# Performance work log

Measured on AMD Instinct MI355X. Metric: run time of the kernel, lower is better.

Reference implementation:

```python
import jax, jax.numpy as jnp
import numpy as np

EPS = 1e-5  # BatchNorm eps


def _bn_relu(x, g, b, m, v):
    # inference-mode BatchNorm2d over channel axis 1, then ReLU
    inv = g / jnp.sqrt(v + EPS)
    return jax.nn.relu(x * inv[None, :, None, None] + (b - m * inv)[None, :, None, None])


def setup_inputs() -> dict:
    key = jax.random.key(0)
    ks = jax.random.split(key, 16)
    B, C, N, K = 8, 64, 16384, 16
    mlp = (128, 64, 64)
    inp = {
        "src_xyz": jax.random.normal(ks[0], (B, 3, N, K), jnp.float32),
        "tgt_xyz": jax.random.normal(ks[1], (B, 3, N), jnp.float32),
        "feature": jax.random.normal(ks[2], (B, C, N, K), jnp.float32),
    }
    prev = C + 4  # use_relation adds diff_xyz(3) + distance(1)
    i = 3
    for li, co in enumerate(mlp, 1):
        scale = (6.0 / (prev + co)) ** 0.5  # xavier_uniform
        inp[f"W{li}"] = jax.random.uniform(ks[i], (co, prev), jnp.float32, -scale, scale)
        inp[f"g{li}"] = jnp.ones((co,), jnp.float32)
        inp[f"b{li}"] = jnp.zeros((co,), jnp.float32)
        inp[f"m{li}"] = jnp.zeros((co,), jnp.float32)
        inp[f"v{li}"] = jnp.ones((co,), jnp.float32)
        prev = co
        i += 1
    return inp


def reference(src_xyz, tgt_xyz, feature,
              W1, g1, b1, m1, v1,
              W2, g2, b2, m2, v2,
              W3, g3, b3, m3, v3):
    d = 3  # NOTE: original code slices the NEIGHBOR dim to :3 (faithful quirk)
    diff = src_xyz[:, :, :, :d] - tgt_xyz[:, :, :, None]      # (B,3,N,3)
    dist = jnp.sum(diff * diff, axis=1, keepdims=True)        # (B,1,N,3)
    x = jnp.concatenate([feature[:, :, :, :d], diff, dist], axis=1)  # (B,C+4,N,3)
    for (W, g, b, m, v) in ((W1, g1, b1, m1, v1), (W2, g2, b2, m2, v2), (W3, g3, b3, m3, v3)):
        x = jnp.einsum('oc,bcnk->bonk', W, x)  # 1x1 conv (shared MLP)
        x = _bn_relu(x, g, b, m, v)
    return jnp.sum(x, axis=3)  # reduction='sum' over neighbor dim -> (B,64,N)
```

## Files before the change

### kernel.cpp

```cpp
#include <hip/hip_runtime.h>


typedef __attribute__((ext_vector_type(8))) short short8v;
typedef __attribute__((ext_vector_type(4))) float f32x4;

#define BN_EPS 1e-5f

__device__ __forceinline__ unsigned short f2bf(float f) {
    union { float f; unsigned u; } U; U.f = f;
    unsigned r = U.u + 0x7FFFu + ((U.u >> 16) & 1u);
    return (unsigned short)(r >> 16);
}

union FragU { uint4 u; short8v s; uint2 h[2]; };


__global__ __launch_bounds__(256) void fa_pack(
    const float* __restrict__ W1, const float* __restrict__ g1, const float* __restrict__ b1,
    const float* __restrict__ m1, const float* __restrict__ v1,
    const float* __restrict__ W2, const float* __restrict__ g2, const float* __restrict__ b2,
    const float* __restrict__ m2, const float* __restrict__ v2,
    const float* __restrict__ W3, const float* __restrict__ g3, const float* __restrict__ b3,
    const float* __restrict__ m3, const float* __restrict__ v3,
    char* __restrict__ ws)
{
    const int id = blockIdx.x * 256 + threadIdx.x;
    if (id < 1536) {
        const int lane = id & 63, frag = id >> 6;
        const int ct = frag / 3, ks = frag - 3 * ct;
        const int o  = ct * 16 + (lane & 15);
        const int kb = ks * 32 + (lane >> 4) * 8;
        unsigned short h[8];
        #pragma unroll
        for (int j = 0; j < 8; ++j) {
            const int k = kb + j;
            h[j] = (k < 68) ? f2bf(W1[o * 68 + k]) : (unsigned short)0;
        }
        uint4 pk;
        pk.x = h[0] | (h[1] << 16); pk.y = h[2] | (h[3] << 16);
        pk.z = h[4] | (h[5] << 16); pk.w = h[6] | (h[7] << 16);
        ((uint4*)ws)[id] = pk;
    } else if (id < 2560) {
        const int i2 = id - 1536;
        const int lane = i2 & 63, frag = i2 >> 6;
        const int o  = (frag >> 2) * 16 + (lane & 15);
        const int kb = (frag & 3) * 32 + (lane >> 4) * 8;
        unsigned short h[8];
        #pragma unroll
        for (int j = 0; j < 8; ++j) h[j] = f2bf(W2[o * 128 + kb + j]);
        uint4 pk;
        pk.x = h[0] | (h[1] << 16); pk.y = h[2] | (h[3] << 16);
        pk.z = h[4] | (h[5] << 16); pk.w = h[6] | (h[7] << 16);
        ((uint4*)(ws + 24576))[i2] = pk;
    } else if (id < 3072) {
        const int i3 = id - 2560;
        const int lane = i3 & 63, frag = i3 >> 6;
        const int o  = (frag >> 1) * 16 + (lane & 15);
        const int kb = (frag & 1) * 32 + (lane >> 4) * 8;
        unsigned short h[8];
        #pragma unroll
        for (int j = 0; j < 8; ++j) h[j] = f2bf(W3[o * 64 + kb + j]);
        uint4 pk;
        pk.x = h[0] | (h[1] << 16); pk.y = h[2] | (h[3] << 16);
        pk.z = h[4] | (h[5] << 16); pk.w = h[6] | (h[7] << 16);
        ((uint4*)(ws + 40960))[i3] = pk;
    } else if (id < 3200) {
        const int o = id - 3072;
        const float s = g1[o] * rsqrtf(v1[o] + BN_EPS);
        ((float*)(ws + 49152))[o] = s;
        ((float*)(ws + 49664))[o] = b1[o] - m1[o] * s;
    } else if (id < 3264) {
        const int o = id - 3200;
        const float s = g2[o] * rsqrtf(v2[o] + BN_EPS);
        ((float*)(ws + 50176))[o] = s;
        ((float*)(ws + 50432))[o] = b2[o] - m2[o] * s;
    } else if (id < 3328) {
        const int o = id - 3264;
        const float s = g3[o] * rsqrtf(v3[o] + BN_EPS);
        ((float*)(ws + 50688))[o] = s;
        ((float*)(ws + 50944))[o] = b3[o] - m3[o] * s;
    }
}

__global__ __launch_bounds__(256, 3) void fa_mfma(
    const float* __restrict__ src, const float* __restrict__ tgt,
    const float* __restrict__ feat,
    const char* __restrict__ ws, float* __restrict__ out)
{
    constexpr int N = 16384;
    __shared__ unsigned short SM[192 * 136];
    #define X0V(r, c) SM[(r) * 72 + (c)]
    #define X1V(r, c) SM[(r) * 136 + (c)]

    const int t  = threadIdx.x;
    const int b  = blockIdx.x >> 8;
    const int n0 = (blockIdx.x & 255) << 6;

    {
        const int p  = t & 63;
        const int cg = t >> 6;
        float4 fr[16];
        #pragma unroll
        for (int i = 0; i < 16; ++i) {
            const int c = cg * 16 + i;
            fr[i] = *(const float4*)(feat + ((size_t)(b * 64 + c) * N + n0 + p) * 16);
        }
        float rs0 = 0, rs1 = 0, rs2 = 0, rt0 = 0, rt1 = 0, rt2 = 0;
        const bool rel = t < 192;
        const int rp = t & 63, rk = t >> 6;
        if (rel) {
            const int n = n0 + rp;
            rs0 = src[((b * 3 + 0) * N + n) * 16 + rk]; rt0 = tgt[(b * 3 + 0) * N + n];
            rs1 = src[((b * 3 + 1) * N + n) * 16 + rk]; rt1 = tgt[(b * 3 + 1) * N + n];
            rs2 = src[((b * 3 + 2) * N + n) * 16 + rk]; rt2 = tgt[(b * 3 + 2) * N + n];
        }
        #pragma unroll
        for (int j = 0; j < 4; ++j) {
            const int c0 = cg * 16 + 4 * j;
            const float4 f0 = fr[4 * j + 0], f1 = fr[4 * j + 1];
            const float4 f2 = fr[4 * j + 2], f3 = fr[4 * j + 3];
            uint2 u0, u1, u2;
            u0.x = f2bf(f0.x) | (f2bf(f1.x) << 16); u0.y = f2bf(f2.x) | (f2bf(f3.x) << 16);
            u1.x = f2bf(f0.y) | (f2bf(f1.y) << 16); u1.y = f2bf(f2.y) | (f2bf(f3.y) << 16);
            u2.x = f2bf(f0.z) | (f2bf(f1.z) << 16); u2.y = f2bf(f2.z) | (f2bf(f3.z) << 16);
            *(uint2*)&X0V(0 * 64 + p, c0) = u0;
            *(uint2*)&X0V(1 * 64 + p, c0) = u1;
            *(uint2*)&X0V(2 * 64 + p, c0) = u2;
        }
        if (rel) {
            const float d0 = rs0 - rt0, d1 = rs1 - rt1, d2 = rs2 - rt2;
            const float ds = d0 * d0 + d1 * d1 + d2 * d2;
            uint2 wr; wr.x = f2bf(d0) | (f2bf(d1) << 16); wr.y = f2bf(d2) | (f2bf(ds) << 16);
            *(uint2*)&X0V(rk * 64 + rp, 64) = wr;
        }
    }
    __syncthreads();

    const int w = t >> 6, lane = t & 63, lo = lane & 15, hi = lane >> 4;

    const uint4*  w1f = (const uint4*)ws;
    const uint4*  w2f = (const uint4*)(ws + 24576);
    const uint4*  w3f = (const uint4*)(ws + 40960);
    const float*  s1w = (const float*)(ws + 49152);
    const float*  t1w = (const float*)(ws + 49664);
    const float*  s2w = (const float*)(ws + 50176);
    const float*  t2w = (const float*)(ws + 50432);
    const float*  s3w = (const float*)(ws + 50688);
    const float*  t3w = (const float*)(ws + 50944);

    short8v a1[3][3];
    #pragma unroll
    for (int k = 0; k < 3; ++k) {
        const int row = k * 64 + w * 16 + lo;
        a1[k][0] = *(const short8v*)&X0V(row, hi * 8);
        a1[k][1] = *(const short8v*)&X0V(row, 32 + hi * 8);
        FragU U; U.u.x = 0; U.u.y = 0; U.u.z = 0; U.u.w = 0;
        if (hi == 0) U.h[0] = *(const uint2*)&X0V(row, 64);
        a1[k][2] = U.s;
    }
    __syncthreads();

    #pragma unroll 2
    for (int ct = 0; ct < 8; ++ct) {
        FragU B0, B1, B2;
        B0.u = w1f[(ct * 3 + 0) * 64 + lane];
        B1.u = w1f[(ct * 3 + 1) * 64 + lane];
        B2.u = w1f[(ct * 3 + 2) * 64 + lane];
        const float sc = s1w[ct * 16 + lo];
        const float tb = t1w[ct * 16 + lo];
        #pragma unroll
        for (int k = 0; k < 3; ++k) {
            f32x4 acc = {0.f, 0.f, 0.f, 0.f};
            acc = __builtin_amdgcn_mfma_f32_16x16x32_bf16(a1[k][0], B0.s, acc, 0, 0, 0);
            acc = __builtin_amdgcn_mfma_f32_16x16x32_bf16(a1[k][1], B1.s, acc, 0, 0, 0);
            acc = __builtin_amdgcn_mfma_f32_16x16x32_bf16(a1[k][2], B2.s, acc, 0, 0, 0);
            const int rb = k * 64 + w * 16 + 4 * hi;
            #pragma unroll
            for (int j = 0; j < 4; ++j) {
                const float y = fmaxf(fmaf(sc, acc[j], tb), 0.f);
                X1V(rb + j, ct * 16 + lo) = f2bf(y);
            }
        }
    }

    short8v a2[3][4];
    #pragma unroll
    for (int k = 0; k < 3; ++k) {
        const int row = k * 64 + w * 16 + lo;
        #pragma unroll
        for (int ks = 0; ks < 4; ++ks)
            a2[k][ks] = *(const short8v*)&X1V(row, ks * 32 + hi * 8);
    }
    __syncthreads();

    #pragma unroll 2
    for (int ct = 0; ct < 4; ++ct) {
        FragU B0, B1, B2, B3;
        B0.u = w2f[(ct * 4 + 0) * 64 + lane];
        B1.u = w2f[(ct * 4 + 1) * 64 + lane];
        B2.u = w2f[(ct * 4 + 2) * 64 + lane];
        B3.u = w2f[(ct * 4 + 3) * 64 + lane];
        const float sc = s2w[ct * 16 + lo];
        const float tb = t2w[ct * 16 + lo];
        #pragma unroll
        for (int k = 0; k < 3; ++k) {
            f32x4 acc = {0.f, 0.f, 0.f, 0.f};
            acc = __builtin_amdgcn_mfma_f32_16x16x32_bf16(a2[k][0], B0.s, acc, 0, 0, 0);
            acc = __builtin_amdgcn_mfma_f32_16x16x32_bf16(a2[k][1], B1.s, acc, 0, 0, 0);
            acc = __builtin_amdgcn_mfma_f32_16x16x32_bf16(a2[k][2], B2.s, acc, 0, 0, 0);
            acc = __builtin_amdgcn_mfma_f32_16x16x32_bf16(a2[k][3], B3.s, acc, 0, 0, 0);
            const int rb = k * 64 + w * 16 + 4 * hi;
            #pragma unroll
            for (int j = 0; j < 4; ++j) {
                const float y = fmaxf(fmaf(sc, acc[j], tb), 0.f);
                X0V(rb + j, ct * 16 + lo) = f2bf(y);
            }
        }
    }

    short8v a3[3][2];
    #pragma unroll
    for (int k = 0; k < 3; ++k) {
        const int row = k * 64 + w * 16 + lo;
        a3[k][0] = *(const short8v*)&X0V(row, hi * 8);
        a3[k][1] = *(const short8v*)&X0V(row, 32 + hi * 8);
    }
    #pragma unroll 2
    for (int ct = 0; ct < 4; ++ct) {
        FragU B0, B1;
        B0.u = w3f[(ct * 2 + 0) * 64 + lane];
        B1.u = w3f[(ct * 2 + 1) * 64 + lane];
        const float sc = s3w[ct * 16 + lo];
        const float tb = t3w[ct * 16 + lo];
        f32x4 acc0 = {0.f, 0.f, 0.f, 0.f};
        f32x4 acc1 = {0.f, 0.f, 0.f, 0.f};
        f32x4 acc2 = {0.f, 0.f, 0.f, 0.f};
        acc0 = __builtin_amdgcn_mfma_f32_16x16x32_bf16(a3[0][0], B0.s, acc0, 0, 0, 0);
        acc0 = __builtin_amdgcn_mfma_f32_16x16x32_bf16(a3[0][1], B1.s, acc0, 0, 0, 0);
        acc1 = __builtin_amdgcn_mfma_f32_16x16x32_bf16(a3[1][0], B0.s, acc1, 0, 0, 0);
        acc1 = __builtin_amdgcn_mfma_f32_16x16x32_bf16(a3[1][1], B1.s, acc1, 0, 0, 0);
        acc2 = __builtin_amdgcn_mfma_f32_16x16x32_bf16(a3[2][0], B0.s, acc2, 0, 0, 0);
        acc2 = __builtin_amdgcn_mfma_f32_16x16x32_bf16(a3[2][1], B1.s, acc2, 0, 0, 0);
        float4 r;
        float* rp4 = &r.x;
        #pragma unroll
        for (int j = 0; j < 4; ++j) {
            rp4[j] = fmaxf(fmaf(sc, acc0[j], tb), 0.f)
                   + fmaxf(fmaf(sc, acc1[j], tb), 0.f)
                   + fmaxf(fmaf(sc, acc2[j], tb), 0.f);
        }
        float* op = out + (size_t)(b * 64 + ct * 16 + lo) * N + n0 + w * 16 + 4 * hi;
        *(float4*)op = r;
    }
    #undef X0V
    #undef X1V
}

extern "C" void kernel_launch(void* const* d_in, const int* in_sizes, int n_in,
                              void* d_out, int out_size, void* d_ws, size_t ws_size,
                              hipStream_t stream)
{
    const float* src  = (const float*)d_in[0];
    const float* tgt  = (const float*)d_in[1];
    const float* feat = (const float*)d_in[2];
    const float* W1 = (const float*)d_in[3];
    const float* g1 = (const float*)d_in[4];
    const float* b1 = (const float*)d_in[5];
    const float* m1 = (const float*)d_in[6];
    const float* v1 = (const float*)d_in[7];
    const float* W2 = (const float*)d_in[8];
    const float* g2 = (const float*)d_in[9];
    const float* b2 = (const float*)d_in[10];
    const float* m2 = (const float*)d_in[11];
    const float* v2 = (const float*)d_in[12];
    const float* W3 = (const float*)d_in[13];
    const float* g3 = (const float*)d_in[14];
    const float* b3 = (const float*)d_in[15];
    const float* m3 = (const float*)d_in[16];
    const float* v3 = (const float*)d_in[17];
    float* out = (float*)d_out;
    char* ws = (char*)d_ws;

    hipLaunchKernelGGL(fa_pack, dim3(13), dim3(256), 0, stream,
                       W1, g1, b1, m1, v1, W2, g2, b2, m2, v2, W3, g3, b3, m3, v3, ws);
    hipLaunchKernelGGL(fa_mfma, dim3(8 * 256), dim3(256), 0, stream,
                       src, tgt, feat, ws, out);
}
```

Before: 135.8 us.

## Make MLP kernel persistent over four tiles with register prefetch of next tile

Each block now processes four consecutive 64-point tiles instead of one, so the grid shrinks from 2048 to 512 blocks. Global loads for the next tile are issued into registers before the three MFMA layers of the current tile run, hiding memory latency behind compute. Custom barriers that wait only on LDS traffic replace __syncthreads so the in-flight global loads are not drained. Launch bounds drop from 3 to 2 blocks per CU to make room for the prefetch registers, which lowers occupancy, and 512 blocks may underfill the CUs.

```diff
diff --git a/kernel.cpp b/kernel.cpp
--- a/kernel.cpp
+++ b/kernel.cpp
@@ -5,6 +5,13 @@
 typedef __attribute__((ext_vector_type(4))) float f32x4;
 
 #define BN_EPS 1e-5f
+
+#define BAR_LGKM() do {                                          \
+    __builtin_amdgcn_sched_barrier(0);                           \
+    asm volatile("s_waitcnt lgkmcnt(0)" ::: "memory");           \
+    __builtin_amdgcn_s_barrier();                                \
+    __builtin_amdgcn_sched_barrier(0);                           \
+} while (0)
 
 __device__ __forceinline__ unsigned short f2bf(float f) {
     union { float f; unsigned u; } U; U.f = f;
@@ -82,7 +89,7 @@
     }
 }
 
-__global__ __launch_bounds__(256, 3) void fa_mfma(
+__global__ __launch_bounds__(256, 2) void fa_mfma(
     const float* __restrict__ src, const float* __restrict__ tgt,
     const float* __restrict__ feat,
     const char* __restrict__ ws, float* __restrict__ out)
@@ -92,50 +99,14 @@
     #define X0V(r, c) SM[(r) * 72 + (c)]
     #define X1V(r, c) SM[(r) * 136 + (c)]
 
-    const int t  = threadIdx.x;
-    const int b  = blockIdx.x >> 8;
-    const int n0 = (blockIdx.x & 255) << 6;
-
-    {
-        const int p  = t & 63;
-        const int cg = t >> 6;
-        float4 fr[16];
-        #pragma unroll
-        for (int i = 0; i < 16; ++i) {
-            const int c = cg * 16 + i;
-            fr[i] = *(const float4*)(feat + ((size_t)(b * 64 + c) * N + n0 + p) * 16);
-        }
-        float rs0 = 0, rs1 = 0, rs2 = 0, rt0 = 0, rt1 = 0, rt2 = 0;
-        const bool rel = t < 192;
-        const int rp = t & 63, rk = t >> 6;
-        if (rel) {
-            const int n = n0 + rp;
-            rs0 = src[((b * 3 + 0) * N + n) * 16 + rk]; rt0 = tgt[(b * 3 + 0) * N + n];
-            rs1 = src[((b * 3 + 1) * N + n) * 16 + rk]; rt1 = tgt[(b * 3 + 1) * N + n];
-            rs2 = src[((b * 3 + 2) * N + n) * 16 + rk]; rt2 = tgt[(b * 3 + 2) * N + n];
-        }
-        #pragma unroll
-        for (int j = 0; j < 4; ++j) {
-            const int c0 = cg * 16 + 4 * j;
-            const float4 f0 = fr[4 * j + 0], f1 = fr[4 * j + 1];
-            const float4 f2 = fr[4 * j + 2], f3 = fr[4 * j + 3];
-            uint2 u0, u1, u2;
-            u0.x = f2bf(f0.x) | (f2bf(f1.x) << 16); u0.y = f2bf(f2.x) | (f2bf(f3.x) << 16);
-            u1.x = f2bf(f0.y) | (f2bf(f1.y) << 16); u1.y = f2bf(f2.y) | (f2bf(f3.y) << 16);
-            u2.x = f2bf(f0.z) | (f2bf(f1.z) << 16); u2.y = f2bf(f2.z) | (f2bf(f3.z) << 16);
-            *(uint2*)&X0V(0 * 64 + p, c0) = u0;
-            *(uint2*)&X0V(1 * 64 + p, c0) = u1;
-            *(uint2*)&X0V(2 * 64 + p, c0) = u2;
-        }
-        if (rel) {
-            const float d0 = rs0 - rt0, d1 = rs1 - rt1, d2 = rs2 - rt2;
-            const float ds = d0 * d0 + d1 * d1 + d2 * d2;
-            uint2 wr; wr.x = f2bf(d0) | (f2bf(d1) << 16); wr.y = f2bf(d2) | (f2bf(ds) << 16);
-            *(uint2*)&X0V(rk * 64 + rp, 64) = wr;
-        }
-    }
-    __syncthreads();
-
+    const int t = threadIdx.x;
+    const int b      = blockIdx.x >> 6;
+    const int base_n = (blockIdx.x & 63) << 8;
+
+    const int p  = t & 63;
+    const int cg = t >> 6;
+    const bool rel = t < 192;
+    const int rp = t & 63, rk = t >> 6;
     const int w = t >> 6, lane = t & 63, lo = lane & 15, hi = lane >> 4;
 
     const uint4*  w1f = (const uint4*)ws;
@@ -148,109 +119,161 @@
     const float*  s3w = (const float*)(ws + 50688);
     const float*  t3w = (const float*)(ws + 50944);
 
-    short8v a1[3][3];
-    #pragma unroll
-    for (int k = 0; k < 3; ++k) {
-        const int row = k * 64 + w * 16 + lo;
-        a1[k][0] = *(const short8v*)&X0V(row, hi * 8);
-        a1[k][1] = *(const short8v*)&X0V(row, 32 + hi * 8);
-        FragU U; U.u.x = 0; U.u.y = 0; U.u.z = 0; U.u.w = 0;
-        if (hi == 0) U.h[0] = *(const uint2*)&X0V(row, 64);
-        a1[k][2] = U.s;
-    }
-    __syncthreads();
-
-    #pragma unroll 2
-    for (int ct = 0; ct < 8; ++ct) {
-        FragU B0, B1, B2;
-        B0.u = w1f[(ct * 3 + 0) * 64 + lane];
-        B1.u = w1f[(ct * 3 + 1) * 64 + lane];
-        B2.u = w1f[(ct * 3 + 2) * 64 + lane];
-        const float sc = s1w[ct * 16 + lo];
-        const float tb = t1w[ct * 16 + lo];
+    float4 fr[16];
+    float q0 = 0, q1 = 0, q2 = 0, q3 = 0, q4 = 0, q5 = 0;
+
+    auto issue_loads = [&](int n0s) {
+        #pragma unroll
+        for (int i = 0; i < 16; ++i) {
+            const int c = cg * 16 + i;
+            fr[i] = *(const float4*)(feat + ((size_t)(b * 64 + c) * N + n0s + p) * 16);
+        }
+        if (rel) {
+            const int n = n0s + rp;
+            q0 = src[((b * 3 + 0) * N + n) * 16 + rk]; q3 = tgt[(b * 3 + 0) * N + n];
+            q1 = src[((b * 3 + 1) * N + n) * 16 + rk]; q4 = tgt[(b * 3 + 1) * N + n];
+            q2 = src[((b * 3 + 2) * N + n) * 16 + rk]; q5 = tgt[(b * 3 + 2) * N + n];
+        }
+    };
+
+    issue_loads(base_n);
+
+    #pragma unroll 1
+    for (int tt = 0; tt < 4; ++tt) {
+        const int n0 = base_n + tt * 64;
+
+        BAR_LGKM();
+
+        {
+            #pragma unroll
+            for (int j = 0; j < 4; ++j) {
+                const int c0 = cg * 16 + 4 * j;
+                const float4 f0 = fr[4 * j + 0], f1 = fr[4 * j + 1];
+                const float4 f2 = fr[4 * j + 2], f3 = fr[4 * j + 3];
+                uint2 u0, u1, u2;
+                u0.x = f2bf(f0.x) | (f2bf(f1.x) << 16); u0.y = f2bf(f2.x) | (f2bf(f3.x) << 16);
+                u1.x = f2bf(f0.y) | (f2bf(f1.y) << 16); u1.y = f2bf(f2.y) | (f2bf(f3.y) << 16);
+                u2.x = f2bf(f0.z) | (f2bf(f1.z) << 16); u2.y = f2bf(f2.z) | (f2bf(f3.z) << 16);
+                *(uint2*)&X0V(0 * 64 + p, c0) = u0;
+                *(uint2*)&X0V(1 * 64 + p, c0) = u1;
+                *(uint2*)&X0V(2 * 64 + p, c0) = u2;
+            }
+            if (rel) {
+                const float d0 = q0 - q3, d1 = q1 - q4, d2 = q2 - q5;
+                const float ds = d0 * d0 + d1 * d1 + d2 * d2;
+                uint2 wr; wr.x = f2bf(d0) | (f2bf(d1) << 16); wr.y = f2bf(d2) | (f2bf(ds) << 16);
+                *(uint2*)&X0V(rk * 64 + rp, 64) = wr;
+            }
+        }
+
+        if (tt < 3) issue_loads(n0 + 64);
+
+        BAR_LGKM();
+
+        short8v a1[3][3];
         #pragma unroll
         for (int k = 0; k < 3; ++k) {
-            f32x4 acc = {0.f, 0.f, 0.f, 0.f};
-            acc = __builtin_amdgcn_mfma_f32_16x16x32_bf16(a1[k][0], B0.s, acc, 0, 0, 0);
-            acc = __builtin_amdgcn_mfma_f32_16x16x32_bf16(a1[k][1], B1.s, acc, 0, 0, 0);
-            acc = __builtin_amdgcn_mfma_f32_16x16x32_bf16(a1[k][2], B2.s, acc, 0, 0, 0);
-            const int rb = k * 64 + w * 16 + 4 * hi;
+            const int row = k * 64 + w * 16 + lo;
+            a1[k][0] = *(const short8v*)&X0V(row, hi * 8);
+            a1[k][1] = *(const short8v*)&X0V(row, 32 + hi * 8);
+            FragU U; U.u.x = 0; U.u.y = 0; U.u.z = 0; U.u.w = 0;
+            if (hi == 0) U.h[0] = *(const uint2*)&X0V(row, 64);
+            a1[k][2] = U.s;
+        }
+        BAR_LGKM();
+
+        #pragma unroll 2
+        for (int ct = 0; ct < 8; ++ct) {
+            FragU B0, B1, B2;
+            B0.u = w1f[(ct * 3 + 0) * 64 + lane];
+            B1.u = w1f[(ct * 3 + 1) * 64 + lane];
+            B2.u = w1f[(ct * 3 + 2) * 64 + lane];
+            const float sc = s1w[ct * 16 + lo];
+            const float tb = t1w[ct * 16 + lo];
+            #pragma unroll
+            for (int k = 0; k < 3; ++k) {
+                f32x4 acc = {0.f, 0.f, 0.f, 0.f};
+                acc = __builtin_amdgcn_mfma_f32_16x16x32_bf16(a1[k][0], B0.s, acc, 0, 0, 0);
+                acc = __builtin_amdgcn_mfma_f32_16x16x32_bf16(a1[k][1], B1.s, acc, 0, 0, 0);
+                acc = __builtin_amdgcn_mfma_f32_16x16x32_bf16(a1[k][2], B2.s, acc, 0, 0, 0);
+                const int rb = k * 64 + w * 16 + 4 * hi;
+                #pragma unroll
+                for (int j = 0; j < 4; ++j) {
+                    const float y = fmaxf(fmaf(sc, acc[j], tb), 0.f);
+                    X1V(rb + j, ct * 16 + lo) = f2bf(y);
+                }
+            }
+        }
+
+        short8v a2[3][4];
+        #pragma unroll
+        for (int k = 0; k < 3; ++k) {
+            const int row = k * 64 + w * 16 + lo;
+            #pragma unroll
+            for (int ks = 0; ks < 4; ++ks)
+                a2[k][ks] = *(const short8v*)&X1V(row, ks * 32 + hi * 8);
+        }
+        BAR_LGKM();
+
+        #pragma unroll 2
+        for (int ct = 0; ct < 4; ++ct) {
+            FragU B0, B1, B2, B3;
+            B0.u = w2f[(ct * 4 + 0) * 64 + lane];
+            B1.u = w2f[(ct * 4 + 1) * 64 + lane];
+            B2.u = w2f[(ct * 4 + 2) * 64 + lane];
+            B3.u = w2f[(ct * 4 + 3) * 64 + lane];
+            const float sc = s2w[ct * 16 + lo];
+            const float tb = t2w[ct * 16 + lo];
+            #pragma unroll
+            for (int k = 0; k < 3; ++k) {
+                f32x4 acc = {0.f, 0.f, 0.f, 0.f};
+                acc = __builtin_amdgcn_mfma_f32_16x16x32_bf16(a2[k][0], B0.s, acc, 0, 0, 0);
+                acc = __builtin_amdgcn_mfma_f32_16x16x32_bf16(a2[k][1], B1.s, acc, 0, 0, 0);
+                acc = __builtin_amdgcn_mfma_f32_16x16x32_bf16(a2[k][2], B2.s, acc, 0, 0, 0);
+                acc = __builtin_amdgcn_mfma_f32_16x16x32_bf16(a2[k][3], B3.s, acc, 0, 0, 0);
+                const int rb = k * 64 + w * 16 + 4 * hi;
+                #pragma unroll
+                for (int j = 0; j < 4; ++j) {
+                    const float y = fmaxf(fmaf(sc, acc[j], tb), 0.f);
+                    X0V(rb + j, ct * 16 + lo) = f2bf(y);
+                }
+            }
+        }
+
+        short8v a3[3][2];
+        #pragma unroll
+        for (int k = 0; k < 3; ++k) {
+            const int row = k * 64 + w * 16 + lo;
+            a3[k][0] = *(const short8v*)&X0V(row, hi * 8);
+            a3[k][1] = *(const short8v*)&X0V(row, 32 + hi * 8);
+        }
+        #pragma unroll 2
+        for (int ct = 0; ct < 4; ++ct) {
+            FragU B0, B1;
+            B0.u = w3f[(ct * 2 + 0) * 64 + lane];
+            B1.u = w3f[(ct * 2 + 1) * 64 + lane];
+            const float sc = s3w[ct * 16 + lo];
+            const float tb = t3w[ct * 16 + lo];
+            f32x4 acc0 = {0.f, 0.f, 0.f, 0.f};
+            f32x4 acc1 = {0.f, 0.f, 0.f, 0.f};
+            f32x4 acc2 = {0.f, 0.f, 0.f, 0.f};
+            acc0 = __builtin_amdgcn_mfma_f32_16x16x32_bf16(a3[0][0], B0.s, acc0, 0, 0, 0);
+            acc0 = __builtin_amdgcn_mfma_f32_16x16x32_bf16(a3[0][1], B1.s, acc0, 0, 0, 0);
+            acc1 = __builtin_amdgcn_mfma_f32_16x16x32_bf16(a3[1][0], B0.s, acc1, 0, 0, 0);
+            acc1 = __builtin_amdgcn_mfma_f32_16x16x32_bf16(a3[1][1], B1.s, acc1, 0, 0, 0);
+            acc2 = __builtin_amdgcn_mfma_f32_16x16x32_bf16(a3[2][0], B0.s, acc2, 0, 0, 0);
+            acc2 = __builtin_amdgcn_mfma_f32_16x16x32_bf16(a3[2][1], B1.s, acc2, 0, 0, 0);
+            float4 r;
+            float* rp4 = &r.x;
             #pragma unroll
             for (int j = 0; j < 4; ++j) {
-                const float y = fmaxf(fmaf(sc, acc[j], tb), 0.f);
-                X1V(rb + j, ct * 16 + lo) = f2bf(y);
-            }
-        }
-    }
-
-    short8v a2[3][4];
-    #pragma unroll
-    for (int k = 0; k < 3; ++k) {
-        const int row = k * 64 + w * 16 + lo;
-        #pragma unroll
-        for (int ks = 0; ks < 4; ++ks)
-            a2[k][ks] = *(const short8v*)&X1V(row, ks * 32 + hi * 8);
-    }
-    __syncthreads();
-
-    #pragma unroll 2
-    for (int ct = 0; ct < 4; ++ct) {
-        FragU B0, B1, B2, B3;
-        B0.u = w2f[(ct * 4 + 0) * 64 + lane];
-        B1.u = w2f[(ct * 4 + 1) * 64 + lane];
-        B2.u = w2f[(ct * 4 + 2) * 64 + lane];
-        B3.u = w2f[(ct * 4 + 3) * 64 + lane];
-        const float sc = s2w[ct * 16 + lo];
-        const float tb = t2w[ct * 16 + lo];
-        #pragma unroll
-        for (int k = 0; k < 3; ++k) {
-            f32x4 acc = {0.f, 0.f, 0.f, 0.f};
-            acc = __builtin_amdgcn_mfma_f32_16x16x32_bf16(a2[k][0], B0.s, acc, 0, 0, 0);
-            acc = __builtin_amdgcn_mfma_f32_16x16x32_bf16(a2[k][1], B1.s, acc, 0, 0, 0);
-            acc = __builtin_amdgcn_mfma_f32_16x16x32_bf16(a2[k][2], B2.s, acc, 0, 0, 0);
-            acc = __builtin_amdgcn_mfma_f32_16x16x32_bf16(a2[k][3], B3.s, acc, 0, 0, 0);
-            const int rb = k * 64 + w * 16 + 4 * hi;
-            #pragma unroll
-            for (int j = 0; j < 4; ++j) {
-                const float y = fmaxf(fmaf(sc, acc[j], tb), 0.f);
-                X0V(rb + j, ct * 16 + lo) = f2bf(y);
-            }
-        }
-    }
-
-    short8v a3[3][2];
-    #pragma unroll
-    for (int k = 0; k < 3; ++k) {
-        const int row = k * 64 + w * 16 + lo;
-        a3[k][0] = *(const short8v*)&X0V(row, hi * 8);
-        a3[k][1] = *(const short8v*)&X0V(row, 32 + hi * 8);
-    }
-    #pragma unroll 2
-    for (int ct = 0; ct < 4; ++ct) {
-        FragU B0, B1;
-        B0.u = w3f[(ct * 2 + 0) * 64 + lane];
-        B1.u = w3f[(ct * 2 + 1) * 64 + lane];
-        const float sc = s3w[ct * 16 + lo];
-        const float tb = t3w[ct * 16 + lo];
-        f32x4 acc0 = {0.f, 0.f, 0.f, 0.f};
-        f32x4 acc1 = {0.f, 0.f, 0.f, 0.f};
-        f32x4 acc2 = {0.f, 0.f, 0.f, 0.f};
-        acc0 = __builtin_amdgcn_mfma_f32_16x16x32_bf16(a3[0][0], B0.s, acc0, 0, 0, 0);
-        acc0 = __builtin_amdgcn_mfma_f32_16x16x32_bf16(a3[0][1], B1.s, acc0, 0, 0, 0);
-        acc1 = __builtin_amdgcn_mfma_f32_16x16x32_bf16(a3[1][0], B0.s, acc1, 0, 0, 0);
-        acc1 = __builtin_amdgcn_mfma_f32_16x16x32_bf16(a3[1][1], B1.s, acc1, 0, 0, 0);
-        acc2 = __builtin_amdgcn_mfma_f32_16x16x32_bf16(a3[2][0], B0.s, acc2, 0, 0, 0);
-        acc2 = __builtin_amdgcn_mfma_f32_16x16x32_bf16(a3[2][1], B1.s, acc2, 0, 0, 0);
-        float4 r;
-        float* rp4 = &r.x;
-        #pragma unroll
-        for (int j = 0; j < 4; ++j) {
-            rp4[j] = fmaxf(fmaf(sc, acc0[j], tb), 0.f)
-                   + fmaxf(fmaf(sc, acc1[j], tb), 0.f)
-                   + fmaxf(fmaf(sc, acc2[j], tb), 0.f);
-        }
-        float* op = out + (size_t)(b * 64 + ct * 16 + lo) * N + n0 + w * 16 + 4 * hi;
-        *(float4*)op = r;
+                rp4[j] = fmaxf(fmaf(sc, acc0[j], tb), 0.f)
+                       + fmaxf(fmaf(sc, acc1[j], tb), 0.f)
+                       + fmaxf(fmaf(sc, acc2[j], tb), 0.f);
+            }
+            float* op = out + (size_t)(b * 64 + ct * 16 + lo) * N + n0 + w * 16 + 4 * hi;
+            *(float4*)op = r;
+        }
     }
     #undef X0V
     #undef X1V
@@ -283,6 +306,6 @@
 
     hipLaunchKernelGGL(fa_pack, dim3(13), dim3(256), 0, stream,
                        W1, g1, b1, m1, v1, W2, g2, b2, m2, v2, W3, g3, b3, m3, v3, ws);
-    hipLaunchKernelGGL(fa_mfma, dim3(8 * 256), dim3(256), 0, stream,
+    hipLaunchKernelGGL(fa_mfma, dim3(512), dim3(256), 0, stream,
                        src, tgt, feat, ws, out);
 }
```

After: 153.3 us. 1.13x slower.
